# Kernel optimization log

Measured on AMD Instinct MI355X. Metric: run time of the kernel, lower is better.

Reference implementation:

```python
import jax, jax.numpy as jnp
import numpy as np

LAMBDA = 10.0
BETA = 10.0
W = 5  # window size per axis (5,5,5); padding=2 hardcoded in original
DN = ('NCDHW', 'OIDHW', 'NCDHW')


def box_mean(x):
    """Uniform 5x5x5 box-filter mean with zero padding=2, via separable 1D convs."""
    specs = [((1, 1, W, 1, 1), [(2, 2), (0, 0), (0, 0)]),
             ((1, 1, 1, W, 1), [(0, 0), (2, 2), (0, 0)]),
             ((1, 1, 1, 1, W), [(0, 0), (0, 0), (2, 2)])]
    for kshape, pads in specs:
        k = jnp.full(kshape, 1.0 / W, dtype=x.dtype)
        x = jax.lax.conv_general_dilated(x, k, (1, 1, 1), pads, dimension_numbers=DN)
    return x


def lcc_loss(gt, pred):
    omega = gt.size
    d_gt = gt - box_mean(gt)
    d_pred = pred - box_mean(pred)
    num = jnp.square(jnp.sum(d_gt * d_pred))
    den = jnp.sum(jnp.square(d_gt)) * jnp.sum(jnp.square(d_pred))
    den = jnp.maximum(den, 1e-5)
    return -(1.0 / omega) * (num / den)


def reg_field_loss(reg_gt, reg_pred):
    omega = reg_gt.size
    return jnp.sqrt(jnp.sum(jnp.square(reg_pred - reg_gt))) / omega


def tversky_loss2(seg_gt, seg_pred):
    den = jnp.maximum(jnp.sum(seg_gt + seg_pred), 1e-5)
    return -0.5 * jnp.sum(2.0 * seg_gt * seg_pred) / den


def setup_inputs() -> dict:
    key = jax.random.key(0)
    ks = jax.random.split(key, 10)
    shp_f = (2, 3, 128, 128, 128)
    shp_i = (2, 1, 128, 128, 128)
    return {
        'F_0': jax.random.normal(ks[0], shp_f, jnp.float32),
        'F_0g': jax.random.normal(ks[1], shp_f, jnp.float32),
        'I_0': jax.random.uniform(ks[2], shp_i, jnp.float32),
        'I_0R': jax.random.uniform(ks[3], shp_i, jnp.float32),
        'I_1': jax.random.uniform(ks[4], shp_i, jnp.float32),
        'I_1R': jax.random.uniform(ks[5], shp_i, jnp.float32),
        'S_0': jax.random.uniform(ks[6], shp_i, jnp.float32),
        'S_0g': jax.random.uniform(ks[7], shp_i, jnp.float32),
        'S_1': jax.random.uniform(ks[8], shp_i, jnp.float32),
        'S_1g': jax.random.uniform(ks[9], shp_i, jnp.float32),
    }


def reference(F_0, F_0g, I_0, I_0R, I_1, I_1R, S_0, S_0g, S_1, S_1g):
    return (reg_field_loss(F_0, F_0g)
            + LAMBDA * (lcc_loss(I_0, I_0R) + lcc_loss(I_1, I_1R))
            + BETA * (tversky_loss2(S_0, S_0g) + tversky_loss2(S_1, S_1g)))
```

## Files before the change

### kernel.cpp

```cpp
#include <hip/hip_runtime.h>
#include <math.h>

#define VOL   (128*128*128)
#define PLANE (128*128)

#define LCC_BLOCKS   1024
#define SQ_BLOCKS    1024
#define TV_BLOCKS    256
#define TOTAL_BLOCKS (LCC_BLOCKS + SQ_BLOCKS + 2 * TV_BLOCKS)

__device__ __forceinline__ void bar_lds_only() {
    asm volatile("s_waitcnt lgkmcnt(0)" ::: "memory");
    __builtin_amdgcn_s_barrier();
}


__device__ __forceinline__ double wave_reduce_d(double v) {
    #pragma unroll
    for (int off = 32; off > 0; off >>= 1)
        v += __shfl_down(v, off, 64);
    return v;
}

__device__ __forceinline__ void block_reduce1_atomic(double a, double* dst) {
    __shared__ double s1[4];
    int lane = threadIdx.x & 63;
    int wave = threadIdx.x >> 6;
    a = wave_reduce_d(a);
    if (lane == 0) s1[wave] = a;
    __syncthreads();
    if (threadIdx.x == 0) {
        double A = s1[0] + s1[1] + s1[2] + s1[3];
        atomicAdd(&dst[0], A);
    }
}

__device__ __forceinline__ void block_reduce2_atomic(double a, double b, double* dst) {
    __shared__ double s2[2][4];
    int lane = threadIdx.x & 63;
    int wave = threadIdx.x >> 6;
    a = wave_reduce_d(a);
    b = wave_reduce_d(b);
    if (lane == 0) { s2[0][wave] = a; s2[1][wave] = b; }
    __syncthreads();
    if (threadIdx.x == 0) {
        atomicAdd(&dst[0], s2[0][0] + s2[0][1] + s2[0][2] + s2[0][3]);
        atomicAdd(&dst[1], s2[1][0] + s2[1][1] + s2[1][2] + s2[1][3]);
    }
}

__device__ __forceinline__ void block_reduce3_atomic(double a, double b, double c, double* dst) {
    __shared__ double s3[3][4];
    int lane = threadIdx.x & 63;
    int wave = threadIdx.x >> 6;
    a = wave_reduce_d(a);
    b = wave_reduce_d(b);
    c = wave_reduce_d(c);
    if (lane == 0) { s3[0][wave] = a; s3[1][wave] = b; s3[2][wave] = c; }
    __syncthreads();
    if (threadIdx.x == 0) {
        atomicAdd(&dst[0], s3[0][0] + s3[0][1] + s3[0][2] + s3[0][3]);
        atomicAdd(&dst[1], s3[1][0] + s3[1][1] + s3[1][2] + s3[1][3]);
        atomicAdd(&dst[2], s3[2][0] + s3[2][1] + s3[2][2] + s3[2][3]);
    }
}


__global__ void zero_ws_kernel(double* ws) {
    if (threadIdx.x < 16) ws[threadIdx.x] = 0.0;
}


__global__ __launch_bounds__(256) void mega_kernel(
    const float* __restrict__ F0,  const float* __restrict__ F0g,
    const float* __restrict__ I0,  const float* __restrict__ I0R,
    const float* __restrict__ I1,  const float* __restrict__ I1R,
    const float* __restrict__ S0,  const float* __restrict__ S0g,
    const float* __restrict__ S1,  const float* __restrict__ S1g,
    double* __restrict__ ws)
{
    int b = blockIdx.x;
    int tid = threadIdx.x;

    if (b < LCC_BLOCKS) {
        __shared__ float ybuf[2 * 8 * 128];
        __shared__ float dbuf[8 * 128];

        int L = (b & 7) * 128 + (b >> 3);

        int pair = L >> 9;
        int r  = L & 511;
        int y0 = (r & 15) << 3;
        int z0 = ((r >> 4) & 15) << 3;
        int n  = r >> 8;

        const float* gt = pair ? I1  : I0;
        const float* pr = pair ? I1R : I0R;
        double* dst = ws + (pair ? 4 : 1);

        int x = tid & 127;
        int g = tid >> 7;
        const float* V = (g ? pr : gt) + (size_t)n * VOL;

        float a1 = 0.f, a2 = 0.f, a3 = 0.f;
        float ps[5][8];
        float cent1[8], cent2[8];
        float vp[3][12];
        float ybk[8];

        float* yb = ybuf + g * 1024;

        #pragma unroll
        for (int s = 0; s < 2; ++s) {
            int zp = z0 - 2 + s;
            bool zin = (zp >= 0);
            #pragma unroll
            for (int j = 0; j < 12; ++j) {
                int gy = y0 - 2 + j;
                vp[s][j] = (zin && gy >= 0 && gy < 128)
                             ? V[(size_t)zp * PLANE + (size_t)gy * 128 + x] : 0.0f;
            }
        }

        #pragma unroll
        for (int it = 0; it < 12; ++it) {
            const int cur = it % 3;
            const int nxt = (it + 2) % 3;

            if (it < 10) {
                int zq = z0 + it;
                bool zok = (zq < 128);
                #pragma unroll
                for (int j = 0; j < 12; ++j) {
                    int gy = y0 - 2 + j;
                    vp[nxt][j] = (zok && gy >= 0 && gy < 128)
                                   ? V[(size_t)zq * PLANE + (size_t)gy * 128 + x] : 0.0f;
                }
            }

            #pragma unroll
            for (int k = 0; k < 8; ++k) {
                float s = vp[cur][k] + vp[cur][k+1] + vp[cur][k+2]
                        + vp[cur][k+3] + vp[cur][k+4];
                ybk[k] = s;
                yb[k * 128 + x] = s;
            }

            bar_lds_only();

            #pragma unroll
            for (int k = 0; k < 8; ++k) {
                float s = ybk[k];
                if (x >= 2)   s += yb[k * 128 + x - 2];
                if (x >= 1)   s += yb[k * 128 + x - 1];
                if (x <= 126) s += yb[k * 128 + x + 1];
                if (x <= 125) s += yb[k * 128 + x + 2];
                ps[it % 5][k] = s;
            }

            float d[8];
            if (it >= 4) {
                #pragma unroll
                for (int k = 0; k < 8; ++k) {
                    float m = (ps[0][k] + ps[1][k] + ps[2][k] + ps[3][k] + ps[4][k])
                              * (1.0f / 125.0f);
                    d[k] = cent2[k] - m;
                }
                if (g) {
                    #pragma unroll
                    for (int k = 0; k < 8; ++k) {
                        dbuf[k * 128 + x] = d[k];
                        a3 += d[k] * d[k];
                    }
                }
            }

            bar_lds_only();

            if (it >= 4 && g == 0) {
                #pragma unroll
                for (int k = 0; k < 8; ++k) {
                    float dp = dbuf[k * 128 + x];
                    a1 += d[k] * dp;
                    a2 += d[k] * d[k];
                }
            }

            #pragma unroll
            for (int k = 0; k < 8; ++k) { cent2[k] = cent1[k]; cent1[k] = vp[cur][k + 2]; }
        }
        block_reduce3_atomic((double)a1, (double)a2, (double)a3, dst);

    } else if (b < LCC_BLOCKS + SQ_BLOCKS) {
        int bid = b - LCC_BLOCKS;
        const float4* A = (const float4*)F0;
        const float4* B = (const float4*)F0g;
        int n4 = 12582912 / 4;
        int idx = bid * 256 + tid;
        int stride = SQ_BLOCKS * 256;
        float acc = 0.f;
        #pragma unroll 4
        for (int i = idx; i < n4; i += stride) {
            float4 xx = A[i], yy = B[i];
            float d0 = yy.x - xx.x, d1 = yy.y - xx.y;
            float d2 = yy.z - xx.z, d3 = yy.w - xx.w;
            acc += (d0 * d0 + d1 * d1) + (d2 * d2 + d3 * d3);
        }
        block_reduce1_atomic((double)acc, &ws[0]);

    } else {
        int bid = b - (LCC_BLOCKS + SQ_BLOCKS);
        int pair = bid >= TV_BLOCKS;
        bid -= pair ? TV_BLOCKS : 0;
        const float4* Gp = (const float4*)(pair ? S1 : S0);
        const float4* Pp = (const float4*)(pair ? S1g : S0g);
        double* dst = ws + (pair ? 9 : 7);
        int n4 = 4194304 / 4;
        int idx = bid * 256 + tid;
        int stride = TV_BLOCKS * 256;
        float asum = 0.f, aprod = 0.f;
        #pragma unroll 4
        for (int i = idx; i < n4; i += stride) {
            float4 xx = Gp[i], yy = Pp[i];
            asum  += (xx.x + yy.x) + (xx.y + yy.y) + (xx.z + yy.z) + (xx.w + yy.w);
            aprod += (xx.x * yy.x + xx.y * yy.y) + (xx.z * yy.z + xx.w * yy.w);
        }
        block_reduce2_atomic((double)asum, (double)aprod, dst);
    }
}

__global__ void finalize_kernel(const double* __restrict__ ws, float* out) {
    if (threadIdx.x == 0 && blockIdx.x == 0) {
        double reg = sqrt(ws[0]) / 12582912.0;

        double num0 = ws[1] * ws[1];
        double den0 = ws[2] * ws[3];
        if (den0 < 1e-5) den0 = 1e-5;
        double l0 = -(1.0 / 4194304.0) * (num0 / den0);

        double num1 = ws[4] * ws[4];
        double den1 = ws[5] * ws[6];
        if (den1 < 1e-5) den1 = 1e-5;
        double l1 = -(1.0 / 4194304.0) * (num1 / den1);

        double td0 = ws[7]; if (td0 < 1e-5) td0 = 1e-5;
        double t0 = -ws[8] / td0;
        double td1 = ws[9]; if (td1 < 1e-5) td1 = 1e-5;
        double t1 = -ws[10] / td1;

        out[0] = (float)(reg + 10.0 * (l0 + l1) + 10.0 * (t0 + t1));
    }
}


extern "C" void kernel_launch(void* const* d_in, const int* in_sizes, int n_in,
                              void* d_out, int out_size, void* d_ws, size_t ws_size,
                              hipStream_t stream) {
    double* ws = (double*)d_ws;
    float* out = (float*)d_out;

    const float* F0  = (const float*)d_in[0];
    const float* F0g = (const float*)d_in[1];
    const float* I0  = (const float*)d_in[2];
    const float* I0R = (const float*)d_in[3];
    const float* I1  = (const float*)d_in[4];
    const float* I1R = (const float*)d_in[5];
    const float* S0  = (const float*)d_in[6];
    const float* S0g = (const float*)d_in[7];
    const float* S1  = (const float*)d_in[8];
    const float* S1g = (const float*)d_in[9];

    zero_ws_kernel<<<1, 64, 0, stream>>>(ws);
    mega_kernel<<<TOTAL_BLOCKS, 256, 0, stream>>>(F0, F0g, I0, I0R, I1, I1R,
                                                  S0, S0g, S1, S1g, ws);
    finalize_kernel<<<1, 64, 0, stream>>>(ws, out);
}
```

Measured before the change: 260.8 us.

## Halve LCC z-tile depth and interleave block types across the grid

```diff
diff --git a/kernel.cpp b/kernel.cpp
--- a/kernel.cpp
+++ b/kernel.cpp
@@ -4,10 +4,11 @@
 #define VOL   (128*128*128)
 #define PLANE (128*128)
 
-#define LCC_BLOCKS   1024
+#define LCC_BLOCKS   2048
 #define SQ_BLOCKS    1024
 #define TV_BLOCKS    256
-#define TOTAL_BLOCKS (LCC_BLOCKS + SQ_BLOCKS + 2 * TV_BLOCKS)
+#define GROUPS       512
+#define TOTAL_BLOCKS (GROUPS * 7)
 
 __device__ __forceinline__ void bar_lds_only() {
     asm volatile("s_waitcnt lgkmcnt(0)" ::: "memory");
@@ -71,7 +72,7 @@
 }
 
 
-__global__ __launch_bounds__(256) void mega_kernel(
+__global__ __launch_bounds__(256, 8) void mega_kernel(
     const float* __restrict__ F0,  const float* __restrict__ F0g,
     const float* __restrict__ I0,  const float* __restrict__ I0R,
     const float* __restrict__ I1,  const float* __restrict__ I1R,
@@ -82,17 +83,20 @@
     int b = blockIdx.x;
     int tid = threadIdx.x;
 
-    if (b < LCC_BLOCKS) {
+    int grp = b / 7;
+    int c   = b - grp * 7;
+
+    if (c < 4) {
         __shared__ float ybuf[2 * 8 * 128];
         __shared__ float dbuf[8 * 128];
 
-        int L = (b & 7) * 128 + (b >> 3);
-
-        int pair = L >> 9;
-        int r  = L & 511;
-        int y0 = (r & 15) << 3;
-        int z0 = ((r >> 4) & 15) << 3;
-        int n  = r >> 8;
+        int l = grp * 4 + c;
+        int pair = l >> 10;
+        int r  = l & 1023;
+        int n  = r >> 9;
+        int s  = r & 511;
+        int y0 = (s & 15) << 3;
+        int z0 = (s >> 4) << 2;
 
         const float* gt = pair ? I1  : I0;
         const float* pr = pair ? I1R : I0R;
@@ -111,23 +115,23 @@
         float* yb = ybuf + g * 1024;
 
         #pragma unroll
-        for (int s = 0; s < 2; ++s) {
-            int zp = z0 - 2 + s;
+        for (int sdx = 0; sdx < 2; ++sdx) {
+            int zp = z0 - 2 + sdx;
             bool zin = (zp >= 0);
             #pragma unroll
             for (int j = 0; j < 12; ++j) {
                 int gy = y0 - 2 + j;
-                vp[s][j] = (zin && gy >= 0 && gy < 128)
-                             ? V[(size_t)zp * PLANE + (size_t)gy * 128 + x] : 0.0f;
+                vp[sdx][j] = (zin && gy >= 0 && gy < 128)
+                               ? V[(size_t)zp * PLANE + (size_t)gy * 128 + x] : 0.0f;
             }
         }
 
         #pragma unroll
-        for (int it = 0; it < 12; ++it) {
+        for (int it = 0; it < 8; ++it) {
             const int cur = it % 3;
             const int nxt = (it + 2) % 3;
 
-            if (it < 10) {
+            if (it < 6) {
                 int zq = z0 + it;
                 bool zok = (zq < 128);
                 #pragma unroll
@@ -140,22 +144,22 @@
 
             #pragma unroll
             for (int k = 0; k < 8; ++k) {
-                float s = vp[cur][k] + vp[cur][k+1] + vp[cur][k+2]
-                        + vp[cur][k+3] + vp[cur][k+4];
-                ybk[k] = s;
-                yb[k * 128 + x] = s;
+                float sv = vp[cur][k] + vp[cur][k+1] + vp[cur][k+2]
+                         + vp[cur][k+3] + vp[cur][k+4];
+                ybk[k] = sv;
+                yb[k * 128 + x] = sv;
             }
 
             bar_lds_only();
 
             #pragma unroll
             for (int k = 0; k < 8; ++k) {
-                float s = ybk[k];
-                if (x >= 2)   s += yb[k * 128 + x - 2];
-                if (x >= 1)   s += yb[k * 128 + x - 1];
-                if (x <= 126) s += yb[k * 128 + x + 1];
-                if (x <= 125) s += yb[k * 128 + x + 2];
-                ps[it % 5][k] = s;
+                float sv = ybk[k];
+                if (x >= 2)   sv += yb[k * 128 + x - 2];
+                if (x >= 1)   sv += yb[k * 128 + x - 1];
+                if (x <= 126) sv += yb[k * 128 + x + 1];
+                if (x <= 125) sv += yb[k * 128 + x + 2];
+                ps[it % 5][k] = sv;
             }
 
             float d[8];
@@ -191,8 +195,8 @@
         }
         block_reduce3_atomic((double)a1, (double)a2, (double)a3, dst);
 
-    } else if (b < LCC_BLOCKS + SQ_BLOCKS) {
-        int bid = b - LCC_BLOCKS;
+    } else if (c < 6) {
+        int bid = grp * 2 + (c - 4);
         const float4* A = (const float4*)F0;
         const float4* B = (const float4*)F0g;
         int n4 = 12582912 / 4;
@@ -209,7 +213,7 @@
         block_reduce1_atomic((double)acc, &ws[0]);
 
     } else {
-        int bid = b - (LCC_BLOCKS + SQ_BLOCKS);
+        int bid = grp;
         int pair = bid >= TV_BLOCKS;
         bid -= pair ? TV_BLOCKS : 0;
         const float4* Gp = (const float4*)(pair ? S1 : S0);
```

After: 331.6 us. +27.2%, slower.
